# Kernel optimization log

Hardware: AMD Instinct MI355X
Metric: run time of the kernel (lower is better)

The kernel has to match this reference:

```python
import jax, jax.numpy as jnp
import numpy as np

N_TEST = 16384
NUM_CLASSES = 1000
TEMPERATURE = 2.0


def setup_inputs() -> dict:
    key = jax.random.key(0)
    ks = jax.random.split(key, 6)
    mk = lambda k: jax.random.normal(k, (N_TEST, NUM_CLASSES), dtype=jnp.float32)
    return {
        "outputs1": mk(ks[0]),
        "outputs2": mk(ks[1]),
        "outputs3": mk(ks[2]),
        "outputs4": mk(ks[3]),
        "mimic": mk(ks[4]),
        "targets": jax.random.randint(ks[5], (N_TEST,), 0, NUM_CLASSES, dtype=jnp.int64),
        "n_test": N_TEST,
    }


def _margin(o, targets):
    # top-2 reduction replaces the full descending sort (same top-2 values)
    top2, _ = jax.lax.top_k(o, 2)                                   # [n, 2]
    tgt_val = jnp.take_along_axis(o, targets[:, None], axis=1)[:, 0]  # [n]
    # margin = (max - second_max) only when target is the argmax value, else 0
    return jnp.where(top2[:, 0] == tgt_val, top2[:, 0] - top2[:, 1], jnp.zeros((), o.dtype))


def reference(outputs1, outputs2, outputs3, outputs4, mimic, targets, n_test):
    outs = (outputs1, outputs2, outputs3, outputs4, mimic)
    preds = jnp.stack([_margin(o, targets) for o in outs], axis=1)  # [n, 5]
    out_threshold = jax.nn.softmax(preds / TEMPERATURE, axis=1)
    max_preds = jnp.max(jnp.stack((outputs1, outputs2, outputs3, outputs4), axis=0))
    return max_preds, out_threshold
```

## Files before the change

### kernel.cpp

```cpp
#include <hip/hip_runtime.h>
#include <math.h>

#define NCLS  1000
#define NV4   250
#define NROWS 16384
#define INV_TEMP 0.5f
#define NEG_INF (-INFINITY)

__device__ __forceinline__ void merge2(float& a1, float& a2, float b1, float b2) {
    const float mn = fminf(a1, b1);
    a1 = fmaxf(a1, b1);
    a2 = fmaxf(mn, fmaxf(a2, b2));
}

__global__ __launch_bounds__(256) void margins_kernel(
    const float* __restrict__ o1, const float* __restrict__ o2,
    const float* __restrict__ o3, const float* __restrict__ o4,
    const float* __restrict__ mim, const int* __restrict__ targets,
    float* __restrict__ ws_margin, float* __restrict__ blockmax)
{
    const int lane = threadIdx.x & 63;
    const int wid  = threadIdx.x >> 6;
    const int pair = blockIdx.x * 4 + wid;
    const int row  = pair / 5;
    const int mat  = pair - row * 5;
    __shared__ float smax[4];

    const float* base = (mat == 0) ? o1 : (mat == 1) ? o2 : (mat == 2) ? o3
                      : (mat == 3) ? o4 : mim;
    const float*  rowp = base + (size_t)row * NCLS;
    const float4* p4   = (const float4*)rowp;

    const int tgt = targets[row];
    const float tv = rowp[tgt];
    float4 v0 = p4[lane];
    float4 v1 = p4[64  + lane];
    float4 v2 = p4[128 + lane];
    float4 v3 = p4[(lane < 58) ? (192 + lane) : 249];
    if (lane >= 58) v3 = make_float4(NEG_INF, NEG_INF, NEG_INF, NEG_INF);

    float t1[4], t2[4];
    const float4 vv[4] = {v0, v1, v2, v3};
    #pragma unroll
    for (int i = 0; i < 4; ++i) {
        const float hi1 = fmaxf(vv[i].x, vv[i].y), lo1 = fminf(vv[i].x, vv[i].y);
        const float hi2 = fmaxf(vv[i].z, vv[i].w), lo2 = fminf(vv[i].z, vv[i].w);
        t1[i] = fmaxf(hi1, hi2);
        t2[i] = fmaxf(fminf(hi1, hi2), fmaxf(lo1, lo2));
    }
    merge2(t1[0], t2[0], t1[1], t2[1]);
    merge2(t1[2], t2[2], t1[3], t2[3]);
    merge2(t1[0], t2[0], t1[2], t2[2]);
    float m1 = t1[0], m2 = t2[0];

    #pragma unroll
    for (int off = 32; off >= 1; off >>= 1) {
        const float q1 = __shfl_xor(m1, off, 64);
        const float q2 = __shfl_xor(m2, off, 64);
        merge2(m1, m2, q1, q2);
    }

    if (lane == 0) {
        ws_margin[pair] = (m1 == tv) ? (m1 - m2) : 0.0f;
        smax[wid] = (mat < 4) ? m1 : NEG_INF;
    }
    __syncthreads();
    if (threadIdx.x == 0)
        blockmax[blockIdx.x] =
            fmaxf(fmaxf(smax[0], smax[1]), fmaxf(smax[2], smax[3]));
}

__global__ __launch_bounds__(256) void softmax_kernel(
    const float* __restrict__ ws_margin, const float* __restrict__ blockmax,
    float* __restrict__ out, float* __restrict__ stage2, int nblocks)
{
    const int row = blockIdx.x * 256 + threadIdx.x;
    if (row < NROWS) {
        const float* pr = ws_margin + (size_t)row * 5;
        const float p0 = pr[0] * INV_TEMP, p1 = pr[1] * INV_TEMP,
                    p2 = pr[2] * INV_TEMP, p3 = pr[3] * INV_TEMP,
                    p4 = pr[4] * INV_TEMP;
        const float pm = fmaxf(fmaxf(fmaxf(p0, p1), fmaxf(p2, p3)), p4);
        const float e0 = expf(p0 - pm), e1 = expf(p1 - pm), e2 = expf(p2 - pm),
                    e3 = expf(p3 - pm), e4 = expf(p4 - pm);
        const float inv = 1.0f / (e0 + e1 + e2 + e3 + e4);
        float* b = out + 1 + (size_t)row * 5;
        b[0] = e0 * inv; b[1] = e1 * inv; b[2] = e2 * inv;
        b[3] = e3 * inv; b[4] = e4 * inv;
    }

    float m = NEG_INF;
    for (int i = blockIdx.x * 320 + threadIdx.x, e = min((int)((blockIdx.x + 1) * 320), nblocks);
         i < e; i += 256)
        m = fmaxf(m, blockmax[i]);
    #pragma unroll
    for (int off = 32; off >= 1; off >>= 1)
        m = fmaxf(m, __shfl_xor(m, off, 64));
    __shared__ float s[4];
    const int lane = threadIdx.x & 63, wid = threadIdx.x >> 6;
    if (lane == 0) s[wid] = m;
    __syncthreads();
    if (threadIdx.x == 0)
        stage2[blockIdx.x] = fmaxf(fmaxf(s[0], s[1]), fmaxf(s[2], s[3]));
}

__global__ __launch_bounds__(64) void final_max_kernel(
    const float* __restrict__ stage2, int n, float* __restrict__ out)
{
    float m = (threadIdx.x < n) ? stage2[threadIdx.x] : NEG_INF;
    #pragma unroll
    for (int off = 32; off >= 1; off >>= 1)
        m = fmaxf(m, __shfl_xor(m, off, 64));
    if (threadIdx.x == 0) out[0] = m;
}

extern "C" void kernel_launch(void* const* d_in, const int* in_sizes, int n_in,
                              void* d_out, int out_size, void* d_ws, size_t ws_size,
                              hipStream_t stream) {
    const float* o1  = (const float*)d_in[0];
    const float* o2  = (const float*)d_in[1];
    const float* o3  = (const float*)d_in[2];
    const float* o4  = (const float*)d_in[3];
    const float* mim = (const float*)d_in[4];
    const int*   tgt = (const int*)d_in[5];

    float* out = (float*)d_out;
    float* ws_margin = (float*)d_ws;
    const int nblocks = (NROWS * 5) / 4;
    float* blockmax = ws_margin + NROWS * 5;
    float* stage2   = blockmax + nblocks;

    margins_kernel<<<nblocks, 256, 0, stream>>>(o1, o2, o3, o4, mim, tgt,
                                                ws_margin, blockmax);
    softmax_kernel<<<64, 256, 0, stream>>>(ws_margin, blockmax, out, stage2, nblocks);
    final_max_kernel<<<1, 64, 0, stream>>>(stage2, 64, out);
}
```

Measured before the change: 291.9 us.

## Fuse margin and softmax into one row-per-wave kernel covering all five matrices

Each wave now loads the same row from all five matrices, computes the five top-2 margins and the softmax in registers, and writes the output directly. This removes the workspace round trip for margins, one kernel launch, and the scattered per-row target load, since the target value is taken from registers with a shuffle. A single 1024-thread block then reduces the per-row maxima. In exchange, each wave holds about 20 float4 values in flight, which raises register pressure and may lower occupancy, and the grid has fewer blocks.

```diff
diff --git a/kernel.cpp b/kernel.cpp
--- a/kernel.cpp
+++ b/kernel.cpp
@@ -2,7 +2,6 @@
 #include <math.h>
 
 #define NCLS  1000
-#define NV4   250
 #define NROWS 16384
 #define INV_TEMP 0.5f
 #define NEG_INF (-INFINITY)
@@ -13,32 +12,10 @@
     a2 = fmaxf(mn, fmaxf(a2, b2));
 }
 
-__global__ __launch_bounds__(256) void margins_kernel(
-    const float* __restrict__ o1, const float* __restrict__ o2,
-    const float* __restrict__ o3, const float* __restrict__ o4,
-    const float* __restrict__ mim, const int* __restrict__ targets,
-    float* __restrict__ ws_margin, float* __restrict__ blockmax)
+__device__ __forceinline__ void top2_wave(const float4& v0, const float4& v1,
+                                          const float4& v2, const float4& v3,
+                                          float& m1, float& m2)
 {
-    const int lane = threadIdx.x & 63;
-    const int wid  = threadIdx.x >> 6;
-    const int pair = blockIdx.x * 4 + wid;
-    const int row  = pair / 5;
-    const int mat  = pair - row * 5;
-    __shared__ float smax[4];
-
-    const float* base = (mat == 0) ? o1 : (mat == 1) ? o2 : (mat == 2) ? o3
-                      : (mat == 3) ? o4 : mim;
-    const float*  rowp = base + (size_t)row * NCLS;
-    const float4* p4   = (const float4*)rowp;
-
-    const int tgt = targets[row];
-    const float tv = rowp[tgt];
-    float4 v0 = p4[lane];
-    float4 v1 = p4[64  + lane];
-    float4 v2 = p4[128 + lane];
-    float4 v3 = p4[(lane < 58) ? (192 + lane) : 249];
-    if (lane >= 58) v3 = make_float4(NEG_INF, NEG_INF, NEG_INF, NEG_INF);
-
     float t1[4], t2[4];
     const float4 vv[4] = {v0, v1, v2, v3};
     #pragma unroll
@@ -51,67 +28,120 @@
     merge2(t1[0], t2[0], t1[1], t2[1]);
     merge2(t1[2], t2[2], t1[3], t2[3]);
     merge2(t1[0], t2[0], t1[2], t2[2]);
-    float m1 = t1[0], m2 = t2[0];
-
+    m1 = t1[0]; m2 = t2[0];
     #pragma unroll
     for (int off = 32; off >= 1; off >>= 1) {
         const float q1 = __shfl_xor(m1, off, 64);
         const float q2 = __shfl_xor(m2, off, 64);
         merge2(m1, m2, q1, q2);
     }
-
-    if (lane == 0) {
-        ws_margin[pair] = (m1 == tv) ? (m1 - m2) : 0.0f;
-        smax[wid] = (mat < 4) ? m1 : NEG_INF;
-    }
-    __syncthreads();
-    if (threadIdx.x == 0)
-        blockmax[blockIdx.x] =
-            fmaxf(fmaxf(smax[0], smax[1]), fmaxf(smax[2], smax[3]));
 }
 
-__global__ __launch_bounds__(256) void softmax_kernel(
-    const float* __restrict__ ws_margin, const float* __restrict__ blockmax,
-    float* __restrict__ out, float* __restrict__ stage2, int nblocks)
+__device__ __forceinline__ float extract_tv(const float4& v0, const float4& v1,
+                                            const float4& v2, const float4& v3,
+                                            int tgt)
 {
-    const int row = blockIdx.x * 256 + threadIdx.x;
-    if (row < NROWS) {
-        const float* pr = ws_margin + (size_t)row * 5;
-        const float p0 = pr[0] * INV_TEMP, p1 = pr[1] * INV_TEMP,
-                    p2 = pr[2] * INV_TEMP, p3 = pr[3] * INV_TEMP,
-                    p4 = pr[4] * INV_TEMP;
-        const float pm = fmaxf(fmaxf(fmaxf(p0, p1), fmaxf(p2, p3)), p4);
-        const float e0 = expf(p0 - pm), e1 = expf(p1 - pm), e2 = expf(p2 - pm),
-                    e3 = expf(p3 - pm), e4 = expf(p4 - pm);
-        const float inv = 1.0f / (e0 + e1 + e2 + e3 + e4);
-        float* b = out + 1 + (size_t)row * 5;
-        b[0] = e0 * inv; b[1] = e1 * inv; b[2] = e2 * inv;
-        b[3] = e3 * inv; b[4] = e4 * inv;
+    const int q = tgt >> 2, comp = tgt & 3, chunk = q >> 6, src = q & 63;
+    const float4 sel = (chunk == 0) ? v0 : (chunk == 1) ? v1
+                     : (chunk == 2) ? v2 : v3;
+    const float c = (comp == 0) ? sel.x : (comp == 1) ? sel.y
+                  : (comp == 2) ? sel.z : sel.w;
+    return __shfl(c, src, 64);
+}
+
+__global__ __launch_bounds__(256) void fused_margin_softmax(
+    const float* __restrict__ o1, const float* __restrict__ o2,
+    const float* __restrict__ o3, const float* __restrict__ o4,
+    const float* __restrict__ mim, const int* __restrict__ targets,
+    float* __restrict__ out, float* __restrict__ wavemax)
+{
+    const int lane = threadIdx.x & 63;
+    const int row  = blockIdx.x * 4 + (threadIdx.x >> 6);
+    const int i3   = (lane < 58) ? (192 + lane) : 249;
+
+    const float4* pa = (const float4*)(o1  + (size_t)row * NCLS);
+    const float4* pb = (const float4*)(o2  + (size_t)row * NCLS);
+    const float4* pc = (const float4*)(o3  + (size_t)row * NCLS);
+    const float4* pd = (const float4*)(o4  + (size_t)row * NCLS);
+    const float4* pe = (const float4*)(mim + (size_t)row * NCLS);
+
+    float4 a0 = pa[lane], a1 = pa[64 + lane], a2 = pa[128 + lane], a3 = pa[i3];
+    float4 b0 = pb[lane], b1 = pb[64 + lane], b2 = pb[128 + lane], b3 = pb[i3];
+    float4 c0 = pc[lane], c1 = pc[64 + lane], c2 = pc[128 + lane], c3 = pc[i3];
+    float4 d0 = pd[lane], d1 = pd[64 + lane], d2 = pd[128 + lane], d3 = pd[i3];
+    float4 e0 = pe[lane], e1 = pe[64 + lane], e2 = pe[128 + lane], e3 = pe[i3];
+    const int tgt = targets[row];
+
+    if (lane >= 58) {
+        const float4 n4 = make_float4(NEG_INF, NEG_INF, NEG_INF, NEG_INF);
+        a3 = n4; b3 = n4; c3 = n4; d3 = n4; e3 = n4;
     }
 
+    float m1, m2, tv, rowmax;
+    float g0, g1, g2, g3, g4;
+
+    tv = extract_tv(a0, a1, a2, a3, tgt);
+    top2_wave(a0, a1, a2, a3, m1, m2);
+    g0 = (m1 == tv) ? (m1 - m2) : 0.0f;
+    rowmax = m1;
+
+    tv = extract_tv(b0, b1, b2, b3, tgt);
+    top2_wave(b0, b1, b2, b3, m1, m2);
+    g1 = (m1 == tv) ? (m1 - m2) : 0.0f;
+    rowmax = fmaxf(rowmax, m1);
+
+    tv = extract_tv(c0, c1, c2, c3, tgt);
+    top2_wave(c0, c1, c2, c3, m1, m2);
+    g2 = (m1 == tv) ? (m1 - m2) : 0.0f;
+    rowmax = fmaxf(rowmax, m1);
+
+    tv = extract_tv(d0, d1, d2, d3, tgt);
+    top2_wave(d0, d1, d2, d3, m1, m2);
+    g3 = (m1 == tv) ? (m1 - m2) : 0.0f;
+    rowmax = fmaxf(rowmax, m1);
+
+    tv = extract_tv(e0, e1, e2, e3, tgt);
+    top2_wave(e0, e1, e2, e3, m1, m2);
+    g4 = (m1 == tv) ? (m1 - m2) : 0.0f;
+
+    const float q0 = g0 * INV_TEMP, q1 = g1 * INV_TEMP, q2 = g2 * INV_TEMP,
+                q3 = g3 * INV_TEMP, q4 = g4 * INV_TEMP;
+    const float pm = fmaxf(fmaxf(fmaxf(q0, q1), fmaxf(q2, q3)), q4);
+    const float x0 = expf(q0 - pm), x1 = expf(q1 - pm), x2 = expf(q2 - pm),
+                x3 = expf(q3 - pm), x4 = expf(q4 - pm);
+    const float inv = 1.0f / (x0 + x1 + x2 + x3 + x4);
+
+    if (lane < 5) {
+        const float r = (lane == 0) ? x0 : (lane == 1) ? x1 : (lane == 2) ? x2
+                      : (lane == 3) ? x3 : x4;
+        out[1 + (size_t)row * 5 + lane] = r * inv;
+    }
+    if (lane == 5) wavemax[row] = rowmax;
+}
+
+__global__ __launch_bounds__(1024) void final_max_kernel(
+    const float* __restrict__ wavemax, float* __restrict__ out)
+{
+    const float4* w4 = (const float4*)wavemax;
     float m = NEG_INF;
-    for (int i = blockIdx.x * 320 + threadIdx.x, e = min((int)((blockIdx.x + 1) * 320), nblocks);
-         i < e; i += 256)
-        m = fmaxf(m, blockmax[i]);
+    #pragma unroll
+    for (int i = 0; i < (NROWS / 4) / 1024; ++i) {
+        const float4 v = w4[threadIdx.x + i * 1024];
+        m = fmaxf(fmaxf(fmaxf(m, v.x), v.y), fmaxf(v.z, v.w));
+    }
     #pragma unroll
     for (int off = 32; off >= 1; off >>= 1)
         m = fmaxf(m, __shfl_xor(m, off, 64));
-    __shared__ float s[4];
+    __shared__ float s[16];
     const int lane = threadIdx.x & 63, wid = threadIdx.x >> 6;
     if (lane == 0) s[wid] = m;
     __syncthreads();
-    if (threadIdx.x == 0)
-        stage2[blockIdx.x] = fmaxf(fmaxf(s[0], s[1]), fmaxf(s[2], s[3]));
-}
-
-__global__ __launch_bounds__(64) void final_max_kernel(
-    const float* __restrict__ stage2, int n, float* __restrict__ out)
-{
-    float m = (threadIdx.x < n) ? stage2[threadIdx.x] : NEG_INF;
-    #pragma unroll
-    for (int off = 32; off >= 1; off >>= 1)
-        m = fmaxf(m, __shfl_xor(m, off, 64));
-    if (threadIdx.x == 0) out[0] = m;
+    if (threadIdx.x == 0) {
+        float mm = s[0];
+        #pragma unroll
+        for (int i = 1; i < 16; ++i) mm = fmaxf(mm, s[i]);
+        out[0] = mm;
+    }
 }
 
 extern "C" void kernel_launch(void* const* d_in, const int* in_sizes, int n_in,
@@ -125,13 +155,9 @@
     const int*   tgt = (const int*)d_in[5];
 
     float* out = (float*)d_out;
-    float* ws_margin = (float*)d_ws;
-    const int nblocks = (NROWS * 5) / 4;
-    float* blockmax = ws_margin + NROWS * 5;
-    float* stage2   = blockmax + nblocks;
+    float* wavemax = (float*)d_ws;
 
-    margins_kernel<<<nblocks, 256, 0, stream>>>(o1, o2, o3, o4, mim, tgt,
-                                                ws_margin, blockmax);
-    softmax_kernel<<<64, 256, 0, stream>>>(ws_margin, blockmax, out, stage2, nblocks);
-    final_max_kernel<<<1, 64, 0, stream>>>(stage2, 64, out);
+    fused_margin_softmax<<<NROWS / 4, 256, 0, stream>>>(o1, o2, o3, o4, mim, tgt,
+                                                        out, wavemax);
+    final_max_kernel<<<1, 1024, 0, stream>>>(wavemax, out);
 }
```

New measurement: 292.2 us. No clear change (+0.1%).
